# Kernel optimization log

Hardware: AMD Instinct MI355X
Metric: run time of the kernel (lower is better)

## Reference

```python
import jax, jax.numpy as jnp
import numpy as np

B, LQ, LK, D, NH = 16, 1024, 1024, 160, 8
HD = D // NH
EPS = 1e-5


def _ln(x, g, b):
    m = x.mean(-1, keepdims=True)
    v = ((x - m) ** 2).mean(-1, keepdims=True)
    return (x - m) / jnp.sqrt(v + EPS) * g + b


def _heads(x, L):
    # [B,L,D] -> [B,NH,L,HD]
    return x.reshape(B, L, NH, HD).transpose(0, 2, 1, 3)


def _attn(qh, kh, vh, scale):
    logits = jnp.einsum('bhqd,bhkd->bhqk', qh, kh) * scale
    p = jax.nn.softmax(logits, axis=-1)
    o = jnp.einsum('bhqk,bhkd->bhqd', p, vh)
    return o.transpose(0, 2, 1, 3).reshape(B, -1, D)


def setup_inputs() -> dict:
    key = jax.random.key(0)
    ks = jax.random.split(key, 16)
    s = 0.02
    inp = {
        'q': jax.random.normal(ks[0], (B, LQ, D), jnp.float32),
        'kv': jax.random.normal(ks[1], (B, LK, D), jnp.float32),
        'ln1_g': jnp.ones((D,), jnp.float32), 'ln1_b': jnp.zeros((D,), jnp.float32),
        'sa_in_w': jax.random.normal(ks[2], (3 * D, D), jnp.float32) * s,
        'sa_in_b': jnp.zeros((3 * D,), jnp.float32),
        'sa_out_w': jax.random.normal(ks[3], (D, D), jnp.float32) * s,
        'sa_out_b': jnp.zeros((D,), jnp.float32),
        'ln2_g': jnp.ones((D,), jnp.float32), 'ln2_b': jnp.zeros((D,), jnp.float32),
        'lnkv_g': jnp.ones((D,), jnp.float32), 'lnkv_b': jnp.zeros((D,), jnp.float32),
        'ca_qw': jax.random.normal(ks[4], (D, D), jnp.float32) * s,
        'ca_qb': jnp.zeros((D,), jnp.float32),
        'ca_kw': jax.random.normal(ks[5], (D, D), jnp.float32) * s,
        'ca_kb': jnp.zeros((D,), jnp.float32),
        'ca_vw': jax.random.normal(ks[6], (D, D), jnp.float32) * s,
        'ca_vb': jnp.zeros((D,), jnp.float32),
        'ca_ow': jax.random.normal(ks[7], (D, D), jnp.float32) * s,
        'ca_ob': jnp.zeros((D,), jnp.float32),
        'log_tau': jnp.zeros((1,), jnp.float32),
        'lnf_g': jnp.ones((D,), jnp.float32), 'lnf_b': jnp.zeros((D,), jnp.float32),
        'w1': jax.random.normal(ks[8], (4 * D, D), jnp.float32) * s,
        'b1': jnp.zeros((4 * D,), jnp.float32),
        'w2': jax.random.normal(ks[9], (D, 4 * D), jnp.float32) * s,
        'b2': jnp.zeros((D,), jnp.float32),
    }
    return inp


def reference(q, kv, ln1_g, ln1_b, sa_in_w, sa_in_b, sa_out_w, sa_out_b,
              ln2_g, ln2_b, lnkv_g, lnkv_b, ca_qw, ca_qb, ca_kw, ca_kb,
              ca_vw, ca_vb, ca_ow, ca_ob, log_tau, lnf_g, lnf_b,
              w1, b1, w2, b2):
    # --- self-attention (pre-LN), standard 1/sqrt(hd) scale ---
    qn = _ln(q, ln1_g, ln1_b)
    qkv = qn @ sa_in_w.T + sa_in_b  # [B,LQ,3D]
    sq, sk, sv = jnp.split(qkv, 3, axis=-1)
    sa = _attn(_heads(sq, LQ), _heads(sk, LQ), _heads(sv, LQ), HD ** -0.5)
    sa = sa @ sa_out_w.T + sa_out_b
    q = q + sa  # DropPath is identity in eval

    # --- cross-attention with learnable temperature ---
    qn = _ln(q, ln2_g, ln2_b)
    kvn = _ln(kv, lnkv_g, lnkv_b)
    tau = jnp.minimum(jax.nn.softplus(log_tau) + 0.5, 2.0)  # clamp max=2.0
    scale = (HD ** -0.5) / tau[0]
    qh = _heads(qn @ ca_qw.T + ca_qb, LQ)
    kh = _heads(kvn @ ca_kw.T + ca_kb, LK)
    vh = _heads(kvn @ ca_vw.T + ca_vb, LK)
    ca = _attn(qh, kh, vh, scale) @ ca_ow.T + ca_ob
    q = q + ca

    # --- FFN with exact GELU ---
    h = _ln(q, lnf_g, lnf_b) @ w1.T + b1
    h = jax.nn.gelu(h, approximate=False)
    q = q + (h @ w2.T + b2)
    return q
```

## Files before the change

### kernel.cpp

```cpp
#include <hip/hip_runtime.h>
#include <hip/hip_bf16.h>
#include <math.h>

#define LQN 1024
#define LKN 1024
#define NB 16
#define DM 160
#define NHEADS 8
#define HDIM 20
#define PSTR 88

typedef __attribute__((ext_vector_type(8))) short bf16x8;
typedef __attribute__((ext_vector_type(4))) float f32x4;

__device__ __forceinline__ float bf2f(unsigned short h) {
  union { unsigned int u; float f; } c; c.u = ((unsigned int)h) << 16; return c.f;
}
__device__ __forceinline__ unsigned short f2bf(float f) {
  union { float f; unsigned int u; } c; c.f = f;
  unsigned int lsb = (c.u >> 16) & 1u;
  unsigned int r = c.u + 0x7fffu + lsb;
  return (unsigned short)(r >> 16);
}
__device__ __forceinline__ unsigned int cvtpk(float a, float b) {
  unsigned int r;
  asm("v_cvt_pk_bf16_f32 %0, %1, %2" : "=v"(r) : "v"(a), "v"(b));
  return r;
}
__device__ __forceinline__ float ex2(float x) { return __builtin_amdgcn_exp2f(x); }

template <int CTRL>
__device__ __forceinline__ float dpp_mov(float x) {
  union { float f; int i; } c; c.f = x;
  c.i = __builtin_amdgcn_update_dpp(c.i, c.i, CTRL, 0xf, 0xf, true);
  return c.f;
}
__device__ __forceinline__ float red16_add(float x) {
  x += dpp_mov<0xB1>(x);
  x += dpp_mov<0x4E>(x);
  x += dpp_mov<0x141>(x);
  x += dpp_mov<0x140>(x);
  return x;
}

__global__ void zero_kernel(uint4* __restrict__ p, int n4) {
  int i = blockIdx.x * 256 + threadIdx.x;
  if (i < n4) p[i] = make_uint4(0, 0, 0, 0);
}

struct CvtArgs {
  const float* src[8];
  int cum[9];
};
__global__ void cvt8_kernel(CvtArgs a, unsigned short* __restrict__ dst) {
  int i = blockIdx.x * 256 + threadIdx.x;
  if (i >= 409600) return;
  int s = 0;
#pragma unroll
  for (int t = 0; t < 7; ++t) s += (i >= a.cum[t + 1]) ? 1 : 0;
  dst[i] = f2bf(a.src[s][i - a.cum[s]]);
}

__global__ void ln_kernel(const float* __restrict__ x,
                          const float* __restrict__ g,
                          const float* __restrict__ b,
                          unsigned short* __restrict__ y, int rows) {
  int row = blockIdx.x * 4 + (threadIdx.x >> 6);
  int lane = threadIdx.x & 63;
  const float* xr = x + (size_t)row * DM;
  float a0 = xr[lane];
  float a1 = xr[lane + 64];
  float a2 = (lane < 32) ? xr[lane + 128] : 0.0f;
  float s = a0 + a1 + a2;
#pragma unroll
  for (int m = 1; m < 64; m <<= 1) s += __shfl_xor(s, m);
  float mean = s * (1.0f / DM);
  float d0 = a0 - mean, d1 = a1 - mean, d2 = a2 - mean;
  float vs = d0 * d0 + d1 * d1 + ((lane < 32) ? d2 * d2 : 0.0f);
#pragma unroll
  for (int m = 1; m < 64; m <<= 1) vs += __shfl_xor(vs, m);
  float rstd = rsqrtf(vs * (1.0f / DM) + 1e-5f);
  unsigned short* yr = y + (size_t)row * DM;
  yr[lane]      = f2bf(d0 * rstd * g[lane]      + b[lane]);
  yr[lane + 64] = f2bf(d1 * rstd * g[lane + 64] + b[lane + 64]);
  if (lane < 32)
    yr[lane + 128] = f2bf(d2 * rstd * g[lane + 128] + b[lane + 128]);
}

__global__ __launch_bounds__(256, 4)
void qkv_kernel(const unsigned short* __restrict__ Aq,
                const unsigned short* __restrict__ Akv,
                const unsigned short* __restrict__ Wq,
                const unsigned short* __restrict__ Wk,
                const unsigned short* __restrict__ Wv,
                const float* __restrict__ bq,
                const float* __restrict__ bk,
                const float* __restrict__ bv,
                unsigned short* __restrict__ Qp,
                unsigned short* __restrict__ Kc,
                unsigned short* __restrict__ Vc) {
  int which = blockIdx.y / 3;
  int yt = blockIdx.y % 3;
  const unsigned short* A = (which == 0) ? Aq : Akv;
  const unsigned short* W = (which == 0) ? Wq : (which == 1 ? Wk : Wv);
  const float* bias = (which == 0) ? bq : (which == 1 ? bk : bv);
  int lane = threadIdx.x & 63;
  int wid = threadIdx.x >> 6;
  int wr = wid >> 1, wc = wid & 1;
  int r0 = blockIdx.x * 64 + wr * 32;
  int c0 = yt * 64 + wc * 32;
  if (c0 >= 160) return;
  int lr = lane & 15;
  int ko = (lane >> 4) * 8;
  const unsigned short* Ap0 = A + (size_t)(r0 + lr) * 160 + ko;
  const unsigned short* Ap1 = Ap0 + (size_t)16 * 160;
  const unsigned short* Wp0 = W + (size_t)(c0 + lr) * 160 + ko;
  const unsigned short* Wp1 = Wp0 + (size_t)16 * 160;
  f32x4 acc00 = {0, 0, 0, 0}, acc01 = {0, 0, 0, 0};
  f32x4 acc10 = {0, 0, 0, 0}, acc11 = {0, 0, 0, 0};
#pragma unroll
  for (int k = 0; k < 160; k += 32) {
    bf16x8 a0 = *(const bf16x8*)(Ap0 + k);
    bf16x8 a1 = *(const bf16x8*)(Ap1 + k);
    bf16x8 b0 = *(const bf16x8*)(Wp0 + k);
    bf16x8 b1 = *(const bf16x8*)(Wp1 + k);
    acc00 = __builtin_amdgcn_mfma_f32_16x16x32_bf16(a0, b0, acc00, 0, 0, 0);
    acc01 = __builtin_amdgcn_mfma_f32_16x16x32_bf16(a0, b1, acc01, 0, 0, 0);
    acc10 = __builtin_amdgcn_mfma_f32_16x16x32_bf16(a1, b0, acc10, 0, 0, 0);
    acc11 = __builtin_amdgcn_mfma_f32_16x16x32_bf16(a1, b1, acc11, 0, 0, 0);
  }
  int cA = c0 + lr, cB = c0 + 16 + lr;
  float bc0 = bias[cA];
  float bc1 = bias[cB];
  int rb = (lane >> 4) * 4;
  int b = r0 >> 10;
  int hA = cA / 20, dA = cA % 20;
  int hB = cB / 20, dB = cB % 20;
  if (which == 0) {
    int pcA = hA * 32 + dA, pcB = hB * 32 + dB;
#pragma unroll
    for (int i = 0; i < 2; ++i) {
      f32x4 aA = i ? acc10 : acc00;
      f32x4 aB = i ? acc11 : acc01;
#pragma unroll
      for (int r = 0; r < 4; ++r) {
        int row = r0 + i * 16 + rb + r;
        Qp[(size_t)row * 256 + pcA] = f2bf(aA[r] + bc0);
        Qp[(size_t)row * 256 + pcB] = f2bf(aB[r] + bc1);
      }
    }
  } else if (which == 1) {
    size_t baseA = ((((size_t)(b * 8 + hA)) * 4 + (dA >> 3)) * 1024) * 8 + (dA & 7);
    size_t baseB = ((((size_t)(b * 8 + hB)) * 4 + (dB >> 3)) * 1024) * 8 + (dB & 7);
#pragma unroll
    for (int i = 0; i < 2; ++i) {
      f32x4 aA = i ? acc10 : acc00;
      f32x4 aB = i ? acc11 : acc01;
#pragma unroll
      for (int r = 0; r < 4; ++r) {
        int tok = (r0 & 1023) + i * 16 + rb + r;
        Kc[baseA + (size_t)tok * 8] = f2bf(aA[r] + bc0);
        Kc[baseB + (size_t)tok * 8] = f2bf(aB[r] + bc1);
      }
    }
  } else {
    int base32 = r0 & 1023;
    size_t vbA = (((size_t)(b * 8 + hA) * 128 + (base32 >> 3)) * 32 + dA) * 8;
    size_t vbB = (((size_t)(b * 8 + hB) * 128 + (base32 >> 3)) * 32 + dB) * 8;
#pragma unroll
    for (int i = 0; i < 2; ++i) {
      f32x4 aA = i ? acc10 : acc00;
      f32x4 aB = i ? acc11 : acc01;
#pragma unroll
      for (int j = 0; j < 4; ++j) {
        int s32 = 2 * (rb + j) + i;
        size_t off = (size_t)(s32 >> 3) * 256 + (s32 & 7);
        Vc[vbA + off] = f2bf(aA[j] + bc0);
        Vc[vbB + off] = f2bf(aB[j] + bc1);
      }
    }
  }
}

template <int EPI, int K>
__global__ __launch_bounds__(256, 4)
void gemm_kernel(const unsigned short* __restrict__ A,
                 const unsigned short* __restrict__ W,
                 const float* __restrict__ bias,
                 const float* __restrict__ res,
                 void* __restrict__ outp, int N) {
  int lane = threadIdx.x & 63;
  int wid = threadIdx.x >> 6;
  int wr = wid >> 1, wc = wid & 1;
  int r0 = blockIdx.x * 64 + wr * 32;
  int c0 = blockIdx.y * 64 + wc * 32;
  if (c0 >= N) return;
  int lr = lane & 15;
  int ko = (lane >> 4) * 8;
  const unsigned short* Ap0 = A + (size_t)(r0 + lr) * K + ko;
  const unsigned short* Ap1 = Ap0 + (size_t)16 * K;
  const unsigned short* Wp0 = W + (size_t)(c0 + lr) * K + ko;
  const unsigned short* Wp1 = Wp0 + (size_t)16 * K;
  f32x4 acc00 = {0, 0, 0, 0}, acc01 = {0, 0, 0, 0};
  f32x4 acc10 = {0, 0, 0, 0}, acc11 = {0, 0, 0, 0};
#pragma unroll
  for (int k = 0; k < K; k += 32) {
    bf16x8 a0 = *(const bf16x8*)(Ap0 + k);
    bf16x8 a1 = *(const bf16x8*)(Ap1 + k);
    bf16x8 b0 = *(const bf16x8*)(Wp0 + k);
    bf16x8 b1 = *(const bf16x8*)(Wp1 + k);
    acc00 = __builtin_amdgcn_mfma_f32_16x16x32_bf16(a0, b0, acc00, 0, 0, 0);
    acc01 = __builtin_amdgcn_mfma_f32_16x16x32_bf16(a0, b1, acc01, 0, 0, 0);
    acc10 = __builtin_amdgcn_mfma_f32_16x16x32_bf16(a1, b0, acc10, 0, 0, 0);
    acc11 = __builtin_amdgcn_mfma_f32_16x16x32_bf16(a1, b1, acc11, 0, 0, 0);
  }
  int cA = c0 + lr, cB = c0 + 16 + lr;
  float bc0 = bias[cA];
  float bc1 = bias[cB];
  int rb = (lane >> 4) * 4;
#pragma unroll
  for (int i = 0; i < 2; ++i) {
    f32x4 aA = i ? acc10 : acc00;
    f32x4 aB = i ? acc11 : acc01;
#pragma unroll
    for (int r = 0; r < 4; ++r) {
      int row = r0 + i * 16 + rb + r;
      float v0 = aA[r] + bc0;
      float v1 = aB[r] + bc1;
      if (EPI == 2) {
        v0 = 0.5f * v0 * (1.0f + erff(v0 * 0.70710678118654752f));
        v1 = 0.5f * v1 * (1.0f + erff(v1 * 0.70710678118654752f));
        unsigned short* out = (unsigned short*)outp;
        out[(size_t)row * N + cA] = f2bf(v0);
        out[(size_t)row * N + cB] = f2bf(v1);
      } else {
        float* out = (float*)outp;
        out[(size_t)row * N + cA] = v0 + res[(size_t)row * N + cA];
        out[(size_t)row * N + cB] = v1 + res[(size_t)row * N + cB];
      }
    }
  }
}

__global__ __launch_bounds__(256, 4)
void attn_kernel(const unsigned short* __restrict__ Qp,
                 const unsigned short* __restrict__ Kc,
                 const unsigned short* __restrict__ Vc,
                 unsigned short* __restrict__ O,
                 const float* __restrict__ tau_ptr,
                 float base_scale) {
  __shared__ unsigned short kbuf[2][2048];
  __shared__ unsigned short vbuf[2][2048];
  __shared__ unsigned short plds[4][32 * PSTR];
  int lane = threadIdx.x & 63;
  int wid = threadIdx.x >> 6;
  int bh = blockIdx.x;
  int b = bh >> 3, h = bh & 7;
  int q0 = blockIdx.y * 128 + wid * 32;
  float sc = base_scale;
  if (tau_ptr) {
    float lt = tau_ptr[0];
    float sp = (lt > 20.0f) ? lt : log1pf(expf(lt));
    sc /= fminf(sp + 0.5f, 2.0f);
  }
  float scale = sc * 1.4426950408889634f;
  int lr = lane & 15;
  int g = lane >> 4;
  int ko = g * 8;
  int rb = g * 4;
  const size_t tb = (size_t)b * LQN;
  union { bf16x8 v; unsigned short s[8]; unsigned int u[4]; } fq0, fq1;
  fq0.v = *(const bf16x8*)(Qp + (tb + q0 + lr) * 256 + h * 32 + ko);
  fq1.v = *(const bf16x8*)(Qp + (tb + q0 + 16 + lr) * 256 + h * 32 + ko);
#pragma unroll
  for (int j = 0; j < 4; ++j) {
    fq0.u[j] = cvtpk(bf2f(fq0.s[2 * j]) * scale, bf2f(fq0.s[2 * j + 1]) * scale);
    fq1.u[j] = cvtpk(bf2f(fq1.s[2 * j]) * scale, bf2f(fq1.s[2 * j + 1]) * scale);
  }
  bf16x8 aq0 = fq0.v, aq1 = fq1.v;
  const unsigned short* ksrc = Kc + (((size_t)bh * 4 + wid) * 1024) * 8;
  const unsigned short* vsrc = Vc + (size_t)bh * 32768;
  int sdst = wid * 512 + lane * 8;
  {
    uint4 k0 = *(const uint4*)(ksrc + lane * 8);
    uint4 v0 = *(const uint4*)(vsrc + sdst);
    *(uint4*)(kbuf[0] + sdst) = k0;
    *(uint4*)(vbuf[0] + sdst) = v0;
  }
  __syncthreads();
  int cur = 0;
  unsigned short* pwr = plds[wid] + rb * PSTR + 2 * lr;
  const unsigned short* pra = plds[wid] + lr * PSTR + ko;
  f32x4 o00 = {0, 0, 0, 0}, o01 = {0, 0, 0, 0};
  f32x4 o10 = {0, 0, 0, 0}, o11 = {0, 0, 0, 0};
  f32x4 psum0 = {0, 0, 0, 0}, psum1 = {0, 0, 0, 0};
  const f32x4 zero = {0, 0, 0, 0};
  for (int kt = 0; kt < LKN; kt += 64) {
    int ktn = (kt + 64 < LKN) ? kt + 64 : 0;
    uint4 kn = *(const uint4*)(ksrc + (ktn + lane) * 8);
    uint4 vn = *(const uint4*)(vsrc + ktn * 32 + sdst);
    const unsigned short* kb = kbuf[cur];
    const unsigned short* vbp = vbuf[cur];
    bf16x8 ck0 = *(const bf16x8*)(kb + g * 512 + lr * 8);
    bf16x8 ck1 = *(const bf16x8*)(kb + g * 512 + (16 + lr) * 8);
    bf16x8 ck2 = *(const bf16x8*)(kb + g * 512 + (32 + lr) * 8);
    bf16x8 ck3 = *(const bf16x8*)(kb + g * 512 + (48 + lr) * 8);
    f32x4 s0a = __builtin_amdgcn_mfma_f32_16x16x32_bf16(aq0, ck0, zero, 0, 0, 0);
    f32x4 s1a = __builtin_amdgcn_mfma_f32_16x16x32_bf16(aq0, ck1, zero, 0, 0, 0);
    f32x4 s2a = __builtin_amdgcn_mfma_f32_16x16x32_bf16(aq0, ck2, zero, 0, 0, 0);
    f32x4 s3a = __builtin_amdgcn_mfma_f32_16x16x32_bf16(aq0, ck3, zero, 0, 0, 0);
    f32x4 s0b = __builtin_amdgcn_mfma_f32_16x16x32_bf16(aq1, ck0, zero, 0, 0, 0);
    f32x4 s1b = __builtin_amdgcn_mfma_f32_16x16x32_bf16(aq1, ck1, zero, 0, 0, 0);
    f32x4 s2b = __builtin_amdgcn_mfma_f32_16x16x32_bf16(aq1, ck2, zero, 0, 0, 0);
    f32x4 s3b = __builtin_amdgcn_mfma_f32_16x16x32_bf16(aq1, ck3, zero, 0, 0, 0);
    bf16x8 vb00 = *(const bf16x8*)(vbp + g * 256 + lr * 8);
    bf16x8 vb01 = *(const bf16x8*)(vbp + (4 + g) * 256 + lr * 8);
    bf16x8 vb10 = *(const bf16x8*)(vbp + g * 256 + (16 + lr) * 8);
    bf16x8 vb11 = *(const bf16x8*)(vbp + (4 + g) * 256 + (16 + lr) * 8);
#pragma unroll
    for (int r = 0; r < 4; ++r) {
      float p0 = ex2(s0a[r]);
      float p1 = ex2(s1a[r]);
      float p2 = ex2(s2a[r]);
      float p3 = ex2(s3a[r]);
      psum0[r] += (p0 + p1) + (p2 + p3);
      *(unsigned int*)(pwr + r * PSTR)      = cvtpk(p0, p1);
      *(unsigned int*)(pwr + r * PSTR + 32) = cvtpk(p2, p3);
      float q0v = ex2(s0b[r]);
      float q1v = ex2(s1b[r]);
      float q2v = ex2(s2b[r]);
      float q3v = ex2(s3b[r]);
      psum1[r] += (q0v + q1v) + (q2v + q3v);
      *(unsigned int*)(pwr + (16 + r) * PSTR)      = cvtpk(q0v, q1v);
      *(unsigned int*)(pwr + (16 + r) * PSTR + 32) = cvtpk(q2v, q3v);
    }
    bf16x8 pa0a = *(const bf16x8*)(pra);
    bf16x8 pa1a = *(const bf16x8*)(pra + 32);
    bf16x8 pa0b = *(const bf16x8*)(pra + 16 * PSTR);
    bf16x8 pa1b = *(const bf16x8*)(pra + 16 * PSTR + 32);
    o00 = __builtin_amdgcn_mfma_f32_16x16x32_bf16(pa0a, vb00, o00, 0, 0, 0);
    o00 = __builtin_amdgcn_mfma_f32_16x16x32_bf16(pa1a, vb01, o00, 0, 0, 0);
    o01 = __builtin_amdgcn_mfma_f32_16x16x32_bf16(pa0a, vb10, o01, 0, 0, 0);
    o01 = __builtin_amdgcn_mfma_f32_16x16x32_bf16(pa1a, vb11, o01, 0, 0, 0);
    o10 = __builtin_amdgcn_mfma_f32_16x16x32_bf16(pa0b, vb00, o10, 0, 0, 0);
    o10 = __builtin_amdgcn_mfma_f32_16x16x32_bf16(pa1b, vb01, o10, 0, 0, 0);
    o11 = __builtin_amdgcn_mfma_f32_16x16x32_bf16(pa0b, vb10, o11, 0, 0, 0);
    o11 = __builtin_amdgcn_mfma_f32_16x16x32_bf16(pa1b, vb11, o11, 0, 0, 0);
    *(uint4*)(kbuf[cur ^ 1] + sdst) = kn;
    *(uint4*)(vbuf[cur ^ 1] + sdst) = vn;
    __syncthreads();
    cur ^= 1;
  }
  unsigned short* ob = O + (tb + q0) * DM + h * HDIM;
#pragma unroll
  for (int r = 0; r < 4; ++r) {
    int qr = rb + r;
    float inv0 = 1.0f / red16_add(psum0[r]);
    ob[(size_t)qr * DM + lr] = f2bf(o00[r] * inv0);
    if (lr < 4) ob[(size_t)qr * DM + 16 + lr] = f2bf(o01[r] * inv0);
    float inv1 = 1.0f / red16_add(psum1[r]);
    ob[(size_t)(16 + qr) * DM + lr] = f2bf(o10[r] * inv1);
    if (lr < 4) ob[(size_t)(16 + qr) * DM + 16 + lr] = f2bf(o11[r] * inv1);
  }
}

extern "C" void kernel_launch(void* const* d_in, const int* in_sizes, int n_in,
                              void* d_out, int out_size, void* d_ws, size_t ws_size,
                              hipStream_t stream) {
  (void)in_sizes; (void)n_in; (void)out_size; (void)ws_size;
  const float* q        = (const float*)d_in[0];
  const float* kv       = (const float*)d_in[1];
  const float* ln1_g    = (const float*)d_in[2];
  const float* ln1_b    = (const float*)d_in[3];
  const float* sa_in_w  = (const float*)d_in[4];
  const float* sa_in_b  = (const float*)d_in[5];
  const float* sa_out_w = (const float*)d_in[6];
  const float* sa_out_b = (const float*)d_in[7];
  const float* ln2_g    = (const float*)d_in[8];
  const float* ln2_b    = (const float*)d_in[9];
  const float* lnkv_g   = (const float*)d_in[10];
  const float* lnkv_b   = (const float*)d_in[11];
  const float* ca_qw    = (const float*)d_in[12];
  const float* ca_qb    = (const float*)d_in[13];
  const float* ca_kw    = (const float*)d_in[14];
  const float* ca_kb    = (const float*)d_in[15];
  const float* ca_vw    = (const float*)d_in[16];
  const float* ca_vb    = (const float*)d_in[17];
  const float* ca_ow    = (const float*)d_in[18];
  const float* ca_ob    = (const float*)d_in[19];
  const float* log_tau  = (const float*)d_in[20];
  const float* lnf_g    = (const float*)d_in[21];
  const float* lnf_b    = (const float*)d_in[22];
  const float* w1       = (const float*)d_in[23];
  const float* b1       = (const float*)d_in[24];
  const float* w2       = (const float*)d_in[25];
  const float* b2       = (const float*)d_in[26];

  const int M = NB * LQN;
  char* ws = (char*)d_ws;
  unsigned short* wb   = (unsigned short*)(ws);
  unsigned short* qn   = (unsigned short*)(ws + 1048576);
  unsigned short* sqp  = (unsigned short*)(ws + 6291456);
  unsigned short* skc  = (unsigned short*)(ws + 14680064);
  unsigned short* svc  = (unsigned short*)(ws + 23068672);
  unsigned short* attn = (unsigned short*)(ws + 31457280);
  unsigned short* kvn  = (unsigned short*)(ws + 36700160);
  float*          q1   = (float*)(ws + 41943040);
  float*          q2   = (float*)(ws + 52428800);
  unsigned short* hbuf = (unsigned short*)(ws + 6291456);

  unsigned short* b_sa_in  = wb;
  unsigned short* b_sa_out = wb + 76800;
  unsigned short* b_ca_q   = wb + 102400;
  unsigned short* b_ca_k   = wb + 128000;
  unsigned short* b_ca_v   = wb + 153600;
  unsigned short* b_ca_o   = wb + 179200;
  unsigned short* b_w1     = wb + 204800;
  unsigned short* b_w2     = wb + 307200;

  dim3 blk(256);
  const float isq = 0.22360679774997896f;

  zero_kernel<<<dim3(6144), blk, 0, stream>>>((uint4*)(ws + 6291456), 1572864);

  CvtArgs ca;
  ca.src[0] = sa_in_w;  ca.src[1] = sa_out_w; ca.src[2] = ca_qw; ca.src[3] = ca_kw;
  ca.src[4] = ca_vw;    ca.src[5] = ca_ow;    ca.src[6] = w1;    ca.src[7] = w2;
  int cum[9] = {0, 76800, 102400, 128000, 153600, 179200, 204800, 307200, 409600};
  for (int i = 0; i < 9; ++i) ca.cum[i] = cum[i];
  cvt8_kernel<<<dim3(1600), blk, 0, stream>>>(ca, wb);

  ln_kernel<<<dim3(M / 4), blk, 0, stream>>>(q, ln1_g, ln1_b, qn, M);
  qkv_kernel<<<dim3(M / 64, 9), blk, 0, stream>>>(
      qn, qn, b_sa_in, b_sa_in + 160 * 160, b_sa_in + 320 * 160,
      sa_in_b, sa_in_b + 160, sa_in_b + 320, sqp, skc, svc);
  attn_kernel<<<dim3(NB * NHEADS, LQN / 128), blk, 0, stream>>>(sqp, skc, svc, attn, nullptr, isq);
  gemm_kernel<1, 160><<<dim3(M / 64, 3), blk, 0, stream>>>(attn, b_sa_out, sa_out_b, q, q1, 160);

  ln_kernel<<<dim3(M / 4), blk, 0, stream>>>(q1, ln2_g, ln2_b, qn, M);
  ln_kernel<<<dim3(M / 4), blk, 0, stream>>>(kv, lnkv_g, lnkv_b, kvn, M);
  qkv_kernel<<<dim3(M / 64, 9), blk, 0, stream>>>(
      qn, kvn, b_ca_q, b_ca_k, b_ca_v,
      ca_qb, ca_kb, ca_vb, sqp, skc, svc);
  attn_kernel<<<dim3(NB * NHEADS, LQN / 128), blk, 0, stream>>>(sqp, skc, svc, attn, log_tau, isq);
  gemm_kernel<1, 160><<<dim3(M / 64, 3), blk, 0, stream>>>(attn, b_ca_o, ca_ob, q1, q2, 160);

  ln_kernel<<<dim3(M / 4), blk, 0, stream>>>(q2, lnf_g, lnf_b, qn, M);
  gemm_kernel<2, 160><<<dim3(M / 64, 10), blk, 0, stream>>>(qn, b_w1, b1, nullptr, hbuf, 640);
  gemm_kernel<1, 640><<<dim3(M / 64, 3), blk, 0, stream>>>(hbuf, b_w2, b2, q2, (float*)d_out, 160);
}
```

Baseline: 186.7 us.

## Keep softmax probabilities in registers and get row sums from a ones column in V

Swaps the MFMA operand order for QK^T so the exponentiated scores come out already laid out as the A operand for the PV MFMA. This drops the LDS round-trip for P and the per-row DPP reduction. The softmax denominator now comes from a padding column of V preset to bf16 1.0, which a new init kernel writes, and the V write layout in the projection kernel is permuted to match. Row sums are now accumulated from bf16-rounded probabilities, and the result depends on the V padding staying initialised.

```diff
diff --git a/kernel.cpp b/kernel.cpp
--- a/kernel.cpp
+++ b/kernel.cpp
@@ -8,7 +8,6 @@
 #define DM 160
 #define NHEADS 8
 #define HDIM 20
-#define PSTR 88
 
 typedef __attribute__((ext_vector_type(8))) short bf16x8;
 typedef __attribute__((ext_vector_type(4))) float f32x4;
@@ -29,23 +28,17 @@
 }
 __device__ __forceinline__ float ex2(float x) { return __builtin_amdgcn_exp2f(x); }
 
-template <int CTRL>
-__device__ __forceinline__ float dpp_mov(float x) {
-  union { float f; int i; } c; c.f = x;
-  c.i = __builtin_amdgcn_update_dpp(c.i, c.i, CTRL, 0xf, 0xf, true);
-  return c.f;
-}
-__device__ __forceinline__ float red16_add(float x) {
-  x += dpp_mov<0xB1>(x);
-  x += dpp_mov<0x4E>(x);
-  x += dpp_mov<0x141>(x);
-  x += dpp_mov<0x140>(x);
-  return x;
-}
-
 __global__ void zero_kernel(uint4* __restrict__ p, int n4) {
   int i = blockIdx.x * 256 + threadIdx.x;
   if (i < n4) p[i] = make_uint4(0, 0, 0, 0);
+}
+
+__global__ void vinit_kernel(uint4* __restrict__ p, int n4) {
+  int i = blockIdx.x * 256 + threadIdx.x;
+  if (i < n4) {
+    unsigned int v = ((i & 31) == 20) ? 0x3F803F80u : 0u;
+    p[i] = make_uint4(v, v, v, v);
+  }
 }
 
 struct CvtArgs {
@@ -164,17 +157,18 @@
       }
     }
   } else {
-    int base32 = r0 & 1023;
-    size_t vbA = (((size_t)(b * 8 + hA) * 128 + (base32 >> 3)) * 32 + dA) * 8;
-    size_t vbB = (((size_t)(b * 8 + hB) * 128 + (base32 >> 3)) * 32 + dB) * 8;
+    int base64 = (r0 & 1023) & ~63;
+    int hb = (r0 >> 5) & 1;
+    int g = rb >> 2;
+    size_t vbA = (((size_t)(b * 8 + hA) * 128 + (base64 >> 3)) * 32 + dA) * 8;
+    size_t vbB = (((size_t)(b * 8 + hB) * 128 + (base64 >> 3)) * 32 + dB) * 8;
 #pragma unroll
     for (int i = 0; i < 2; ++i) {
       f32x4 aA = i ? acc10 : acc00;
       f32x4 aB = i ? acc11 : acc01;
 #pragma unroll
       for (int j = 0; j < 4; ++j) {
-        int s32 = 2 * (rb + j) + i;
-        size_t off = (size_t)(s32 >> 3) * 256 + (s32 & 7);
+        size_t off = (size_t)(g + hb * 4) * 256 + i * 4 + j;
         Vc[vbA + off] = f2bf(aA[j] + bc0);
         Vc[vbB + off] = f2bf(aB[j] + bc1);
       }
@@ -251,7 +245,6 @@
                  float base_scale) {
   __shared__ unsigned short kbuf[2][2048];
   __shared__ unsigned short vbuf[2][2048];
-  __shared__ unsigned short plds[4][32 * PSTR];
   int lane = threadIdx.x & 63;
   int wid = threadIdx.x >> 6;
   int bh = blockIdx.x;
@@ -289,11 +282,8 @@
   }
   __syncthreads();
   int cur = 0;
-  unsigned short* pwr = plds[wid] + rb * PSTR + 2 * lr;
-  const unsigned short* pra = plds[wid] + lr * PSTR + ko;
   f32x4 o00 = {0, 0, 0, 0}, o01 = {0, 0, 0, 0};
   f32x4 o10 = {0, 0, 0, 0}, o11 = {0, 0, 0, 0};
-  f32x4 psum0 = {0, 0, 0, 0}, psum1 = {0, 0, 0, 0};
   const f32x4 zero = {0, 0, 0, 0};
   for (int kt = 0; kt < LKN; kt += 64) {
     int ktn = (kt + 64 < LKN) ? kt + 64 : 0;
@@ -305,60 +295,57 @@
     bf16x8 ck1 = *(const bf16x8*)(kb + g * 512 + (16 + lr) * 8);
     bf16x8 ck2 = *(const bf16x8*)(kb + g * 512 + (32 + lr) * 8);
     bf16x8 ck3 = *(const bf16x8*)(kb + g * 512 + (48 + lr) * 8);
-    f32x4 s0a = __builtin_amdgcn_mfma_f32_16x16x32_bf16(aq0, ck0, zero, 0, 0, 0);
-    f32x4 s1a = __builtin_amdgcn_mfma_f32_16x16x32_bf16(aq0, ck1, zero, 0, 0, 0);
-    f32x4 s2a = __builtin_amdgcn_mfma_f32_16x16x32_bf16(aq0, ck2, zero, 0, 0, 0);
-    f32x4 s3a = __builtin_amdgcn_mfma_f32_16x16x32_bf16(aq0, ck3, zero, 0, 0, 0);
-    f32x4 s0b = __builtin_amdgcn_mfma_f32_16x16x32_bf16(aq1, ck0, zero, 0, 0, 0);
-    f32x4 s1b = __builtin_amdgcn_mfma_f32_16x16x32_bf16(aq1, ck1, zero, 0, 0, 0);
-    f32x4 s2b = __builtin_amdgcn_mfma_f32_16x16x32_bf16(aq1, ck2, zero, 0, 0, 0);
-    f32x4 s3b = __builtin_amdgcn_mfma_f32_16x16x32_bf16(aq1, ck3, zero, 0, 0, 0);
+    f32x4 s0 = __builtin_amdgcn_mfma_f32_16x16x32_bf16(ck0, aq0, zero, 0, 0, 0);
+    f32x4 s1 = __builtin_amdgcn_mfma_f32_16x16x32_bf16(ck1, aq0, zero, 0, 0, 0);
+    f32x4 s2 = __builtin_amdgcn_mfma_f32_16x16x32_bf16(ck2, aq0, zero, 0, 0, 0);
+    f32x4 s3 = __builtin_amdgcn_mfma_f32_16x16x32_bf16(ck3, aq0, zero, 0, 0, 0);
+    union { bf16x8 v; unsigned int u[4]; } palo1, palo2, pahi1, pahi2;
+    palo1.u[0] = cvtpk(ex2(s0[0]), ex2(s0[1]));
+    palo1.u[1] = cvtpk(ex2(s0[2]), ex2(s0[3]));
+    palo1.u[2] = cvtpk(ex2(s1[0]), ex2(s1[1]));
+    palo1.u[3] = cvtpk(ex2(s1[2]), ex2(s1[3]));
+    palo2.u[0] = cvtpk(ex2(s2[0]), ex2(s2[1]));
+    palo2.u[1] = cvtpk(ex2(s2[2]), ex2(s2[3]));
+    palo2.u[2] = cvtpk(ex2(s3[0]), ex2(s3[1]));
+    palo2.u[3] = cvtpk(ex2(s3[2]), ex2(s3[3]));
+    s0 = __builtin_amdgcn_mfma_f32_16x16x32_bf16(ck0, aq1, zero, 0, 0, 0);
+    s1 = __builtin_amdgcn_mfma_f32_16x16x32_bf16(ck1, aq1, zero, 0, 0, 0);
+    s2 = __builtin_amdgcn_mfma_f32_16x16x32_bf16(ck2, aq1, zero, 0, 0, 0);
+    s3 = __builtin_amdgcn_mfma_f32_16x16x32_bf16(ck3, aq1, zero, 0, 0, 0);
+    pahi1.u[0] = cvtpk(ex2(s0[0]), ex2(s0[1]));
+    pahi1.u[1] = cvtpk(ex2(s0[2]), ex2(s0[3]));
+    pahi1.u[2] = cvtpk(ex2(s1[0]), ex2(s1[1]));
+    pahi1.u[3] = cvtpk(ex2(s1[2]), ex2(s1[3]));
+    pahi2.u[0] = cvtpk(ex2(s2[0]), ex2(s2[1]));
+    pahi2.u[1] = cvtpk(ex2(s2[2]), ex2(s2[3]));
+    pahi2.u[2] = cvtpk(ex2(s3[0]), ex2(s3[1]));
+    pahi2.u[3] = cvtpk(ex2(s3[2]), ex2(s3[3]));
     bf16x8 vb00 = *(const bf16x8*)(vbp + g * 256 + lr * 8);
     bf16x8 vb01 = *(const bf16x8*)(vbp + (4 + g) * 256 + lr * 8);
     bf16x8 vb10 = *(const bf16x8*)(vbp + g * 256 + (16 + lr) * 8);
     bf16x8 vb11 = *(const bf16x8*)(vbp + (4 + g) * 256 + (16 + lr) * 8);
-#pragma unroll
-    for (int r = 0; r < 4; ++r) {
-      float p0 = ex2(s0a[r]);
-      float p1 = ex2(s1a[r]);
-      float p2 = ex2(s2a[r]);
-      float p3 = ex2(s3a[r]);
-      psum0[r] += (p0 + p1) + (p2 + p3);
-      *(unsigned int*)(pwr + r * PSTR)      = cvtpk(p0, p1);
-      *(unsigned int*)(pwr + r * PSTR + 32) = cvtpk(p2, p3);
-      float q0v = ex2(s0b[r]);
-      float q1v = ex2(s1b[r]);
-      float q2v = ex2(s2b[r]);
-      float q3v = ex2(s3b[r]);
-      psum1[r] += (q0v + q1v) + (q2v + q3v);
-      *(unsigned int*)(pwr + (16 + r) * PSTR)      = cvtpk(q0v, q1v);
-      *(unsigned int*)(pwr + (16 + r) * PSTR + 32) = cvtpk(q2v, q3v);
-    }
-    bf16x8 pa0a = *(const bf16x8*)(pra);
-    bf16x8 pa1a = *(const bf16x8*)(pra + 32);
-    bf16x8 pa0b = *(const bf16x8*)(pra + 16 * PSTR);
-    bf16x8 pa1b = *(const bf16x8*)(pra + 16 * PSTR + 32);
-    o00 = __builtin_amdgcn_mfma_f32_16x16x32_bf16(pa0a, vb00, o00, 0, 0, 0);
-    o00 = __builtin_amdgcn_mfma_f32_16x16x32_bf16(pa1a, vb01, o00, 0, 0, 0);
-    o01 = __builtin_amdgcn_mfma_f32_16x16x32_bf16(pa0a, vb10, o01, 0, 0, 0);
-    o01 = __builtin_amdgcn_mfma_f32_16x16x32_bf16(pa1a, vb11, o01, 0, 0, 0);
-    o10 = __builtin_amdgcn_mfma_f32_16x16x32_bf16(pa0b, vb00, o10, 0, 0, 0);
-    o10 = __builtin_amdgcn_mfma_f32_16x16x32_bf16(pa1b, vb01, o10, 0, 0, 0);
-    o11 = __builtin_amdgcn_mfma_f32_16x16x32_bf16(pa0b, vb10, o11, 0, 0, 0);
-    o11 = __builtin_amdgcn_mfma_f32_16x16x32_bf16(pa1b, vb11, o11, 0, 0, 0);
+    o00 = __builtin_amdgcn_mfma_f32_16x16x32_bf16(palo1.v, vb00, o00, 0, 0, 0);
+    o00 = __builtin_amdgcn_mfma_f32_16x16x32_bf16(palo2.v, vb01, o00, 0, 0, 0);
+    o01 = __builtin_amdgcn_mfma_f32_16x16x32_bf16(palo1.v, vb10, o01, 0, 0, 0);
+    o01 = __builtin_amdgcn_mfma_f32_16x16x32_bf16(palo2.v, vb11, o01, 0, 0, 0);
+    o10 = __builtin_amdgcn_mfma_f32_16x16x32_bf16(pahi1.v, vb00, o10, 0, 0, 0);
+    o10 = __builtin_amdgcn_mfma_f32_16x16x32_bf16(pahi2.v, vb01, o10, 0, 0, 0);
+    o11 = __builtin_amdgcn_mfma_f32_16x16x32_bf16(pahi1.v, vb10, o11, 0, 0, 0);
+    o11 = __builtin_amdgcn_mfma_f32_16x16x32_bf16(pahi2.v, vb11, o11, 0, 0, 0);
     *(uint4*)(kbuf[cur ^ 1] + sdst) = kn;
     *(uint4*)(vbuf[cur ^ 1] + sdst) = vn;
     __syncthreads();
     cur ^= 1;
   }
   unsigned short* ob = O + (tb + q0) * DM + h * HDIM;
+  int psl = (lane & 48) + 4;
 #pragma unroll
   for (int r = 0; r < 4; ++r) {
     int qr = rb + r;
-    float inv0 = 1.0f / red16_add(psum0[r]);
+    float inv0 = 1.0f / __shfl(o01[r], psl, 64);
     ob[(size_t)qr * DM + lr] = f2bf(o00[r] * inv0);
     if (lr < 4) ob[(size_t)qr * DM + 16 + lr] = f2bf(o01[r] * inv0);
-    float inv1 = 1.0f / red16_add(psum1[r]);
+    float inv1 = 1.0f / __shfl(o11[r], psl, 64);
     ob[(size_t)(16 + qr) * DM + lr] = f2bf(o10[r] * inv1);
     if (lr < 4) ob[(size_t)(16 + qr) * DM + 16 + lr] = f2bf(o11[r] * inv1);
   }
@@ -421,7 +408,8 @@
   dim3 blk(256);
   const float isq = 0.22360679774997896f;
 
-  zero_kernel<<<dim3(6144), blk, 0, stream>>>((uint4*)(ws + 6291456), 1572864);
+  zero_kernel<<<dim3(4096), blk, 0, stream>>>((uint4*)(ws + 6291456), 1048576);
+  vinit_kernel<<<dim3(2048), blk, 0, stream>>>((uint4*)(ws + 23068672), 524288);
 
   CvtArgs ca;
   ca.src[0] = sa_in_w;  ca.src[1] = sa_out_w; ca.src[2] = ca_qw; ca.src[3] = ca_kw;
```

Measured after the change: 180.3 us. 3.4% less time.
